# Optimization experiments

Hardware: AMD Instinct MI355X
Metric: run time of the kernel (lower is better)

The kernel has to match this reference:

```python
import jax, jax.numpy as jnp
import numpy as np

B, V, F, H, W = 8, 5023, 9976, 512, 512
L = 5  # lights


def setup_inputs() -> dict:
    key = jax.random.key(0)
    ks = jax.random.split(key, 7)
    return {
        "vertices": jax.random.normal(ks[0], (B, V, 3), jnp.float32),
        "transformed_vertices": jax.random.normal(ks[1], (B, V, 3), jnp.float32),
        "lights": jax.random.normal(ks[2], (B, L, 6), jnp.float32),
        "images": jax.random.uniform(ks[3], (B, 3, H, W), jnp.float32),
        "bary": jax.random.uniform(ks[4], (B, H, W, 3), jnp.float32) + 1e-3,
        "faces": jax.random.randint(ks[5], (F, 3), 0, V),
        "pix_to_face": jax.random.randint(ks[6], (B, H, W), 0, F + 1),  # ==F -> background
    }


def _face_vertices(verts, faces):
    # verts [B,V,3], faces [F,3] -> [B,F,3,3]  (gather)
    return verts[:, faces]


def _vertex_normals(verts, faces):
    # gather face verts, per-face cross products, scatter-add back to vertices
    fv = verts[:, faces]                       # [B,F,3,3]
    v0, v1, v2 = fv[:, :, 0], fv[:, :, 1], fv[:, :, 2]
    n = jnp.zeros_like(verts)
    n = n.at[:, faces[:, 1]].add(jnp.cross(v2 - v1, v0 - v1))
    n = n.at[:, faces[:, 2]].add(jnp.cross(v0 - v2, v1 - v2))
    n = n.at[:, faces[:, 0]].add(jnp.cross(v1 - v0, v2 - v0))
    return n / jnp.maximum(jnp.linalg.norm(n, axis=-1, keepdims=True), 1e-6)


def _add_directionlight(normals, lights):
    # normals [B,N,3], lights [B,L,6] -> shading [B,N,3]
    d = lights[:, :, :3]
    d = d / jnp.maximum(jnp.linalg.norm(d, axis=-1, keepdims=True), 1e-12)
    ndl = jnp.clip(jnp.einsum("bnc,blc->bln", normals, d), 0.0, 1.0)  # [B,L,N]
    return jnp.mean(ndl[..., None] * lights[:, :, None, 3:], axis=1)


def reference(vertices, transformed_vertices, lights, images, bary, faces, pix_to_face):
    sg = jax.lax.stop_gradient
    b, nv, _ = vertices.shape
    nf = faces.shape[0]
    h, w = pix_to_face.shape[1], pix_to_face.shape[2]

    tv = transformed_vertices.at[:, :, 2].add(10.0)

    fverts = _face_vertices(vertices, faces)                 # [B,F,3,3]
    normals = _vertex_normals(vertices, faces)               # [B,V,3]
    fnorm = _face_vertices(normals, faces)                   # [B,F,3,3]
    tnorm = _vertex_normals(tv, faces)
    tfnorm = _face_vertices(tnorm, faces)

    colors = jnp.full((b, nf, 3, 3), 180.0 / 255.0, vertices.dtype)  # face_colors buffer
    uv = jnp.zeros((b, nf, 3, 3), vertices.dtype)                    # face_uvcoords (unused downstream)
    # attribute channels: [0:3]=albedo [3:6]=tfnorm [6:9]=verts [9:12]=fnorm [12:15]=uv
    attrs = jnp.concatenate([colors, sg(tfnorm), sg(fverts), fnorm, uv], axis=-1)  # [B,F,3,15]

    # --- rasterizer interpolation stage ---
    p2f = pix_to_face.reshape(b, -1)                         # [B,HW]
    valid = (p2f < nf).astype(vertices.dtype)[..., None]     # [B,HW,1] alpha channel
    fidx = jnp.minimum(p2f, nf - 1)
    pa = jax.vmap(lambda a, i: a[i])(attrs, fidx)            # [B,HW,3,15]
    bw = bary.reshape(b, -1, 3)
    bw = bw / jnp.sum(bw, axis=-1, keepdims=True)
    interp = jnp.einsum("bpk,bpkc->bpc", bw, pa)             # [B,HW,15]

    albedo = interp[..., 0:3]
    tnormal_map = sg(interp[..., 3:6])
    pos_mask = (tnormal_map[..., 2:3] < 0.15).astype(vertices.dtype)
    normal_images = sg(interp[..., 9:12])
    alpha = sg(valid) * pos_mask                             # [B,HW,1]

    shading = _add_directionlight(normal_images, lights)     # [B,HW,3]
    shaded = albedo * shading

    imgs = images.transpose(0, 2, 3, 1).reshape(b, -1, 3)
    out = shaded * alpha + imgs * (1.0 - alpha)              # [B,HW,3]
    return out.reshape(b, h, w, 3).transpose(0, 3, 1, 2)     # [B,3,H,W]
```

## Files before the change

### kernel.cpp

```cpp
#include <hip/hip_runtime.h>
#include <stdint.h>

namespace {

constexpr int kB = 8;
constexpr int kV = 5023;
constexpr int kF = 9976;
constexpr int kH = 512;
constexpr int kW = 512;
constexpr int kL = 5;
constexpr int kHW = kH * kW;
constexpr int kQ = kHW / 4;
constexpr int kCap = 32;

typedef float nfloat4 __attribute__((ext_vector_type(4)));

__device__ __forceinline__ float h2f(uint32_t u) {
  _Float16 h;
  uint16_t s = (uint16_t)u;
  __builtin_memcpy(&h, &s, 2);
  return (float)h;
}
__device__ __forceinline__ uint32_t f2h(float f) {
  _Float16 h = (_Float16)f;
  uint16_t s;
  __builtin_memcpy(&s, &h, 2);
  return (uint32_t)s;
}

__device__ __forceinline__ void cross3(float ax, float ay, float az,
                                       float bx, float by, float bz,
                                       float& cx, float& cy, float& cz) {
  cx = ay * bz - az * by;
  cy = az * bx - ax * bz;
  cz = ax * by - ay * bx;
}

__global__ void init_kernel(int* __restrict__ cnt,
                            const float* __restrict__ lights,
                            float4* __restrict__ ldir4) {
  int idx = blockIdx.x * blockDim.x + threadIdx.x;
  for (int i = idx; i < kV; i += gridDim.x * blockDim.x) cnt[i] = 0;
  if (idx < kB * kL) {
    float dx = lights[idx * 6 + 0];
    float dy = lights[idx * 6 + 1];
    float dz = lights[idx * 6 + 2];
    float inv = 1.0f / fmaxf(sqrtf(dx * dx + dy * dy + dz * dz), 1e-12f);
    ldir4[idx * 2 + 0] = make_float4(dx * inv, dy * inv, dz * inv, 0.0f);
    ldir4[idx * 2 + 1] =
        make_float4(lights[idx * 6 + 3], lights[idx * 6 + 4], lights[idx * 6 + 5], 0.0f);
  }
}

__global__ void prep_kernel(const float* __restrict__ verts,
                            const float* __restrict__ tverts,
                            const int* __restrict__ faces,
                            int* __restrict__ cnt,
                            int* __restrict__ adj,
                            float4* __restrict__ fn) {
  int idx = blockIdx.x * blockDim.x + threadIdx.x;
  if (idx < kF) {
    int f = idx;
#pragma unroll
    for (int c = 0; c < 3; ++c) {
      int v = faces[f * 3 + c];
      int slot = atomicAdd(&cnt[v], 1);
      if (slot < kCap) adj[v * kCap + slot] = f;
    }
    return;
  }
  idx -= kF;
  if (idx >= kB * kF) return;
  int b = idx / kF;
  int f = idx - b * kF;
  int i0 = faces[f * 3 + 0];
  int i1 = faces[f * 3 + 1];
  int i2 = faces[f * 3 + 2];

  float nx, ny, nz, tx, ty, tz;
  {
    const float* vb = verts + (size_t)b * kV * 3;
    float v0x = vb[i0 * 3 + 0], v0y = vb[i0 * 3 + 1], v0z = vb[i0 * 3 + 2];
    float v1x = vb[i1 * 3 + 0], v1y = vb[i1 * 3 + 1], v1z = vb[i1 * 3 + 2];
    float v2x = vb[i2 * 3 + 0], v2y = vb[i2 * 3 + 1], v2z = vb[i2 * 3 + 2];
    cross3(v1x - v0x, v1y - v0y, v1z - v0z, v2x - v0x, v2y - v0y, v2z - v0z,
           nx, ny, nz);
  }
  {
    const float* vb = tverts + (size_t)b * kV * 3;
    float v0x = vb[i0 * 3 + 0], v0y = vb[i0 * 3 + 1], v0z = vb[i0 * 3 + 2] + 10.0f;
    float v1x = vb[i1 * 3 + 0], v1y = vb[i1 * 3 + 1], v1z = vb[i1 * 3 + 2] + 10.0f;
    float v2x = vb[i2 * 3 + 0], v2y = vb[i2 * 3 + 1], v2z = vb[i2 * 3 + 2] + 10.0f;
    cross3(v1x - v0x, v1y - v0y, v1z - v0z, v2x - v0x, v2y - v0y, v2z - v0z,
           tx, ty, tz);
  }
  fn[(size_t)idx * 2 + 0] = make_float4(nx, ny, nz, tx);
  fn[(size_t)idx * 2 + 1] = make_float4(ty, tz, 0.0f, 0.0f);
}

__global__ void gather_normalize_kernel(const int* __restrict__ cnt,
                                        const int* __restrict__ adj,
                                        const float4* __restrict__ fn,
                                        uint4* __restrict__ vrec) {
  int idx = blockIdx.x * blockDim.x + threadIdx.x;
  if (idx >= kB * kV) return;
  int b = idx / kV;
  int v = idx - b * kV;
  int e = min(cnt[v], kCap);
  float nx = 0.f, ny = 0.f, nz = 0.f, tx = 0.f, ty = 0.f, tzv = 0.f;
  const int* av = adj + v * kCap;
  for (int j = 0; j < e; ++j) {
    int f = av[j];
    size_t k = ((size_t)b * kF + f) * 2;
    float4 a = fn[k];
    float4 c = fn[k + 1];
    nx += a.x;
    ny += a.y;
    nz += a.z;
    tx += a.w;
    ty += c.x;
    tzv += c.y;
  }
  float inv = 1.0f / fmaxf(sqrtf(nx * nx + ny * ny + nz * nz), 1e-6f);
  float invt = 1.0f / fmaxf(sqrtf(tx * tx + ty * ty + tzv * tzv), 1e-6f);
  uint4 r;
  r.x = f2h(nx * inv) | (f2h(ny * inv) << 16);
  r.y = f2h(nz * inv);
  r.z = __float_as_uint(tzv * invt);
  r.w = 0;
  vrec[idx] = r;
}

__global__ void faceattr_kernel(const int* __restrict__ faces,
                                const uint4* __restrict__ vrec,
                                uint4* __restrict__ fattr) {
  int b = blockIdx.x % kB;
  int f = (blockIdx.x / kB) * blockDim.x + threadIdx.x;
  if (f >= kF) return;
  int idx = b * kF + f;
  int i0 = faces[f * 3 + 0];
  int i1 = faces[f * 3 + 1];
  int i2 = faces[f * 3 + 2];
  const uint4* vb = vrec + (size_t)b * kV;
  uint4 r0 = vb[i0];
  uint4 r1 = vb[i1];
  uint4 r2 = vb[i2];
  uint4 w0, w1;
  w0.x = r0.x;
  w0.y = (r0.y & 0xffffu) | (r1.x << 16);
  w0.z = (r1.x >> 16) | ((r1.y & 0xffffu) << 16);
  w0.w = r2.x;
  w1.x = r2.y & 0xffffu;
  w1.y = r0.z;
  w1.z = r1.z;
  w1.w = r2.z;
  fattr[(size_t)idx * 2 + 0] = w0;
  fattr[(size_t)idx * 2 + 1] = w1;
}

__global__ void __launch_bounds__(256) pixel4_kernel(
    const int4* __restrict__ p2f4,
    const float4* __restrict__ bary4,
    const uint4* __restrict__ fattr,
    const float4* __restrict__ ldir4,
    const float4* __restrict__ img4,
    float4* __restrict__ out4) {
  int b = blockIdx.x & 7;
  int q = (blockIdx.x >> 3) * blockDim.x + threadIdx.x;
  size_t g = (size_t)b * kQ + q;

  int4 f4 = p2f4[g];
  float4 w0 = bary4[g * 3 + 0];
  float4 w1 = bary4[g * 3 + 1];
  float4 w2 = bary4[g * 3 + 2];

  int fi[4] = {f4.x, f4.y, f4.z, f4.w};
  float bw[4][3] = {{w0.x, w0.y, w0.z},
                    {w0.w, w1.x, w1.y},
                    {w1.z, w1.w, w2.x},
                    {w2.y, w2.z, w2.w}};

  uint4 A[4], T[4];
  bool valid[4];
#pragma unroll
  for (int k = 0; k < 4; ++k) {
    bool v = fi[k] < kF;
    valid[k] = v;
    int f = v ? fi[k] : (kF - 1);
    size_t base = ((size_t)b * kF + f) * 2;
    A[k] = fattr[base + 0];
    T[k] = fattr[base + 1];
  }

  size_t ibase = (size_t)b * 3 * kQ + q;
  float4 im0 = img4[ibase + 0 * (size_t)kQ];
  float4 im1 = img4[ibase + 1 * (size_t)kQ];
  float4 im2 = img4[ibase + 2 * (size_t)kQ];
  float im[3][4] = {{im0.x, im0.y, im0.z, im0.w},
                    {im1.x, im1.y, im1.z, im1.w},
                    {im2.x, im2.y, im2.z, im2.w}};

  int bu = __builtin_amdgcn_readfirstlane(b);
  const float4* lb4 = ldir4 + (size_t)bu * kL * 2;
  float ld[kL][3], lc[kL][3];
#pragma unroll
  for (int l = 0; l < kL; ++l) {
    float4 d = lb4[l * 2 + 0];
    float4 c = lb4[l * 2 + 1];
    ld[l][0] = d.x;
    ld[l][1] = d.y;
    ld[l][2] = d.z;
    lc[l][0] = c.x;
    lc[l][1] = c.y;
    lc[l][2] = c.z;
  }

  float o[3][4];
#pragma unroll
  for (int k = 0; k < 4; ++k) {
    float b0 = bw[k][0], b1 = bw[k][1], b2 = bw[k][2];
    float inv = 1.0f / (b0 + b1 + b2);
    b0 *= inv;
    b1 *= inv;
    b2 *= inv;
    float n0x = h2f(A[k].x), n0y = h2f(A[k].x >> 16);
    float n0z = h2f(A[k].y), n1x = h2f(A[k].y >> 16);
    float n1y = h2f(A[k].z), n1z = h2f(A[k].z >> 16);
    float n2x = h2f(A[k].w), n2y = h2f(A[k].w >> 16);
    float n2z = h2f(T[k].x);
    float tz0 = __uint_as_float(T[k].y);
    float tz1 = __uint_as_float(T[k].z);
    float tz2 = __uint_as_float(T[k].w);

    float tzi = b0 * tz0 + b1 * tz1 + b2 * tz2;
    bool alpha = valid[k] && (tzi < 0.15f);
    float nx = b0 * n0x + b1 * n1x + b2 * n2x;
    float ny = b0 * n0y + b1 * n1y + b2 * n2y;
    float nz = b0 * n0z + b1 * n1z + b2 * n2z;
    float s0 = 0.f, s1 = 0.f, s2 = 0.f;
#pragma unroll
    for (int l = 0; l < kL; ++l) {
      float d = nx * ld[l][0] + ny * ld[l][1] + nz * ld[l][2];
      d = fminf(fmaxf(d, 0.0f), 1.0f);
      s0 += d * lc[l][0];
      s1 += d * lc[l][1];
      s2 += d * lc[l][2];
    }
    const float kk = (180.0f / 255.0f) / (float)kL;
    o[0][k] = alpha ? kk * s0 : im[0][k];
    o[1][k] = alpha ? kk * s1 : im[1][k];
    o[2][k] = alpha ? kk * s2 : im[2][k];
  }

#pragma unroll
  for (int c = 0; c < 3; ++c) {
    nfloat4 v = {o[c][0], o[c][1], o[c][2], o[c][3]};
    __builtin_nontemporal_store(v, (nfloat4*)&out4[ibase + c * (size_t)kQ]);
  }
}

}

extern "C" void kernel_launch(void* const* d_in, const int* in_sizes, int n_in,
                              void* d_out, int out_size, void* d_ws, size_t ws_size,
                              hipStream_t stream) {
  const float* vertices = (const float*)d_in[0];
  const float* tvertices = (const float*)d_in[1];
  const float* lights = (const float*)d_in[2];
  const float* images = (const float*)d_in[3];
  const float* bary = (const float*)d_in[4];
  const int* faces = (const int*)d_in[5];
  const int* p2f = (const int*)d_in[6];
  float* out = (float*)d_out;

  char* ws = (char*)d_ws;
  int* cnt = (int*)ws;
  ws += ((size_t)kV * sizeof(int) + 15) & ~15ull;
  int* adj = (int*)ws;
  ws += ((size_t)kV * kCap * sizeof(int) + 15) & ~15ull;
  float4* fn = (float4*)ws;
  ws += (size_t)kB * kF * 2 * sizeof(float4);
  uint4* vrec = (uint4*)ws;
  ws += (size_t)kB * kV * sizeof(uint4);
  float4* ldir4 = (float4*)ws;
  ws += (size_t)kB * kL * 2 * sizeof(float4);
  uint4* fattr = (uint4*)ws;

  {
    init_kernel<<<20, 256, 0, stream>>>(cnt, lights, ldir4);
  }
  {
    int n = kF + kB * kF;
    prep_kernel<<<(n + 255) / 256, 256, 0, stream>>>(vertices, tvertices, faces, cnt,
                                                     adj, fn);
  }
  {
    int n = kB * kV;
    gather_normalize_kernel<<<(n + 255) / 256, 256, 0, stream>>>(cnt, adj, fn, vrec);
  }
  {
    int chunks = (kF + 255) / 256;
    faceattr_kernel<<<chunks * kB, 256, 0, stream>>>(faces, vrec, fattr);
  }
  {
    pixel4_kernel<<<(kQ / 256) * kB, 256, 0, stream>>>(
        (const int4*)p2f, (const float4*)bary, fattr, ldir4, (const float4*)images,
        (float4*)out);
  }
}
```

Measured before the change: 48.38 us.

## Stage per-batch vertex records and faces in LDS, drop faceattr kernel

```diff
diff --git a/kernel.cpp b/kernel.cpp
--- a/kernel.cpp
+++ b/kernel.cpp
@@ -12,6 +12,10 @@
 constexpr int kHW = kH * kW;
 constexpr int kQ = kHW / 4;
 constexpr int kCap = 32;
+
+constexpr int kVrecLdsBytes = kV * 12;
+constexpr int kFacesLdsOff = (kVrecLdsBytes + 7) & ~7;
+constexpr int kLdsBytes = kFacesLdsOff + kF * 8;
 
 typedef float nfloat4 __attribute__((ext_vector_type(4)));
 
@@ -131,71 +135,54 @@
   vrec[idx] = r;
 }
 
-__global__ void faceattr_kernel(const int* __restrict__ faces,
-                                const uint4* __restrict__ vrec,
-                                uint4* __restrict__ fattr) {
-  int b = blockIdx.x % kB;
-  int f = (blockIdx.x / kB) * blockDim.x + threadIdx.x;
-  if (f >= kF) return;
-  int idx = b * kF + f;
-  int i0 = faces[f * 3 + 0];
-  int i1 = faces[f * 3 + 1];
-  int i2 = faces[f * 3 + 2];
-  const uint4* vb = vrec + (size_t)b * kV;
-  uint4 r0 = vb[i0];
-  uint4 r1 = vb[i1];
-  uint4 r2 = vb[i2];
-  uint4 w0, w1;
-  w0.x = r0.x;
-  w0.y = (r0.y & 0xffffu) | (r1.x << 16);
-  w0.z = (r1.x >> 16) | ((r1.y & 0xffffu) << 16);
-  w0.w = r2.x;
-  w1.x = r2.y & 0xffffu;
-  w1.y = r0.z;
-  w1.z = r1.z;
-  w1.w = r2.z;
-  fattr[(size_t)idx * 2 + 0] = w0;
-  fattr[(size_t)idx * 2 + 1] = w1;
-}
-
-__global__ void __launch_bounds__(256) pixel4_kernel(
+__global__ void __launch_bounds__(1024) pixel_lds_kernel(
     const int4* __restrict__ p2f4,
     const float4* __restrict__ bary4,
-    const uint4* __restrict__ fattr,
+    const uint4* __restrict__ vrec,
+    const int* __restrict__ faces,
     const float4* __restrict__ ldir4,
     const float4* __restrict__ img4,
     float4* __restrict__ out4) {
+  extern __shared__ char smem[];
+  uint32_t* vlds = (uint32_t*)smem;
+  ushort4* flds = (ushort4*)(smem + kFacesLdsOff);
+
   int b = blockIdx.x & 7;
-  int q = (blockIdx.x >> 3) * blockDim.x + threadIdx.x;
+  int tid = threadIdx.x;
+
+  const uint4* vb = vrec + (size_t)b * kV;
+  for (int i = tid; i < kV; i += 1024) {
+    uint4 r = vb[i];
+    vlds[i * 3 + 0] = r.x;
+    vlds[i * 3 + 1] = r.y;
+    vlds[i * 3 + 2] = r.z;
+  }
+  for (int f = tid; f < kF; f += 1024) {
+    int i0 = faces[f * 3 + 0];
+    int i1 = faces[f * 3 + 1];
+    int i2 = faces[f * 3 + 2];
+    flds[f] = make_ushort4((uint16_t)i0, (uint16_t)i1, (uint16_t)i2, 0);
+  }
+  __syncthreads();
+
+  int q = (blockIdx.x >> 3) * 1024 + tid;
   size_t g = (size_t)b * kQ + q;
 
   int4 f4 = p2f4[g];
   float4 w0 = bary4[g * 3 + 0];
   float4 w1 = bary4[g * 3 + 1];
   float4 w2 = bary4[g * 3 + 2];
+
+  size_t ibase = (size_t)b * 3 * kQ + q;
+  float4 im0 = img4[ibase + 0 * (size_t)kQ];
+  float4 im1 = img4[ibase + 1 * (size_t)kQ];
+  float4 im2 = img4[ibase + 2 * (size_t)kQ];
 
   int fi[4] = {f4.x, f4.y, f4.z, f4.w};
   float bw[4][3] = {{w0.x, w0.y, w0.z},
                     {w0.w, w1.x, w1.y},
                     {w1.z, w1.w, w2.x},
                     {w2.y, w2.z, w2.w}};
-
-  uint4 A[4], T[4];
-  bool valid[4];
-#pragma unroll
-  for (int k = 0; k < 4; ++k) {
-    bool v = fi[k] < kF;
-    valid[k] = v;
-    int f = v ? fi[k] : (kF - 1);
-    size_t base = ((size_t)b * kF + f) * 2;
-    A[k] = fattr[base + 0];
-    T[k] = fattr[base + 1];
-  }
-
-  size_t ibase = (size_t)b * 3 * kQ + q;
-  float4 im0 = img4[ibase + 0 * (size_t)kQ];
-  float4 im1 = img4[ibase + 1 * (size_t)kQ];
-  float4 im2 = img4[ibase + 2 * (size_t)kQ];
   float im[3][4] = {{im0.x, im0.y, im0.z, im0.w},
                     {im1.x, im1.y, im1.z, im1.w},
                     {im2.x, im2.y, im2.z, im2.w}};
@@ -218,25 +205,31 @@
   float o[3][4];
 #pragma unroll
   for (int k = 0; k < 4; ++k) {
+    bool valid = fi[k] < kF;
+    int f = valid ? fi[k] : (kF - 1);
+    ushort4 fv = flds[f];
+
+    uint32_t v0x = vlds[fv.x * 3 + 0], v0y = vlds[fv.x * 3 + 1],
+             v0z = vlds[fv.x * 3 + 2];
+    uint32_t v1x = vlds[fv.y * 3 + 0], v1y = vlds[fv.y * 3 + 1],
+             v1z = vlds[fv.y * 3 + 2];
+    uint32_t v2x = vlds[fv.z * 3 + 0], v2y = vlds[fv.z * 3 + 1],
+             v2z = vlds[fv.z * 3 + 2];
+
     float b0 = bw[k][0], b1 = bw[k][1], b2 = bw[k][2];
     float inv = 1.0f / (b0 + b1 + b2);
     b0 *= inv;
     b1 *= inv;
     b2 *= inv;
-    float n0x = h2f(A[k].x), n0y = h2f(A[k].x >> 16);
-    float n0z = h2f(A[k].y), n1x = h2f(A[k].y >> 16);
-    float n1y = h2f(A[k].z), n1z = h2f(A[k].z >> 16);
-    float n2x = h2f(A[k].w), n2y = h2f(A[k].w >> 16);
-    float n2z = h2f(T[k].x);
-    float tz0 = __uint_as_float(T[k].y);
-    float tz1 = __uint_as_float(T[k].z);
-    float tz2 = __uint_as_float(T[k].w);
-
-    float tzi = b0 * tz0 + b1 * tz1 + b2 * tz2;
-    bool alpha = valid[k] && (tzi < 0.15f);
-    float nx = b0 * n0x + b1 * n1x + b2 * n2x;
-    float ny = b0 * n0y + b1 * n1y + b2 * n2y;
-    float nz = b0 * n0z + b1 * n1z + b2 * n2z;
+
+    float tzi = b0 * __uint_as_float(v0z) + b1 * __uint_as_float(v1z) +
+                b2 * __uint_as_float(v2z);
+    bool alpha = valid && (tzi < 0.15f);
+
+    float nx = b0 * h2f(v0x) + b1 * h2f(v1x) + b2 * h2f(v2x);
+    float ny = b0 * h2f(v0x >> 16) + b1 * h2f(v1x >> 16) + b2 * h2f(v2x >> 16);
+    float nz = b0 * h2f(v0y) + b1 * h2f(v1y) + b2 * h2f(v2y);
+
     float s0 = 0.f, s1 = 0.f, s2 = 0.f;
 #pragma unroll
     for (int l = 0; l < kL; ++l) {
@@ -283,8 +276,13 @@
   uint4* vrec = (uint4*)ws;
   ws += (size_t)kB * kV * sizeof(uint4);
   float4* ldir4 = (float4*)ws;
-  ws += (size_t)kB * kL * 2 * sizeof(float4);
-  uint4* fattr = (uint4*)ws;
+
+  static bool attr_set = false;
+  if (!attr_set) {
+    hipFuncSetAttribute((const void*)pixel_lds_kernel,
+                        hipFuncAttributeMaxDynamicSharedMemorySize, kLdsBytes);
+    attr_set = true;
+  }
 
   {
     init_kernel<<<20, 256, 0, stream>>>(cnt, lights, ldir4);
@@ -299,12 +297,8 @@
     gather_normalize_kernel<<<(n + 255) / 256, 256, 0, stream>>>(cnt, adj, fn, vrec);
   }
   {
-    int chunks = (kF + 255) / 256;
-    faceattr_kernel<<<chunks * kB, 256, 0, stream>>>(faces, vrec, fattr);
-  }
-  {
-    pixel4_kernel<<<(kQ / 256) * kB, 256, 0, stream>>>(
-        (const int4*)p2f, (const float4*)bary, fattr, ldir4, (const float4*)images,
-        (float4*)out);
-  }
-}
+    pixel_lds_kernel<<<(kQ / 1024) * kB, 1024, kLdsBytes, stream>>>(
+        (const int4*)p2f, (const float4*)bary, vrec, faces, ldir4,
+        (const float4*)images, (float4*)out);
+  }
+}
```

Measured after the change: 48.63 us. No clear change (+0.5%).
